# Optimization experiments

Measured on AMD Instinct MI355X. Metric: run time of the kernel, lower is better.

Reference implementation:

```python
import jax, jax.numpy as jnp
import numpy as np

N, F, H, O = 3072, 128, 16, 8  # nodes, in_channels, hidden_channels, out_channels


def setup_inputs() -> dict:
    key = jax.random.key(0)
    ks = jax.random.split(key, 8)
    s = 0.01  # xavier gain=0.01 in original init -> small weights
    return {
        "x": jax.random.normal(ks[0], (N, F), dtype=jnp.float32),
        "edge_index": jax.random.randint(ks[1], (2, N * 32), 0, N, dtype=jnp.int64),
        "node_distances": jax.random.uniform(ks[2], (N, N), dtype=jnp.float32),
        "normalization_matrix": jnp.ones((N, N), dtype=jnp.float32),
        # per-feature MLPs fs[f]: Linear(1,H) -> ReLU -> (Dropout p=0) -> Linear(H,O), stacked over F
        "W1": s * jax.random.normal(ks[3], (F, H), dtype=jnp.float32),
        "b1": jnp.zeros((F, H), dtype=jnp.float32),
        "W2": s * jax.random.normal(ks[4], (F, H, O), dtype=jnp.float32),
        "b2": jnp.zeros((F, O), dtype=jnp.float32),
        # rho MLP: Linear(1,H) -> ReLU -> Linear(H,O) (bias=True since is_graph_task=False)
        "rW1": s * jax.random.normal(ks[5], (H,), dtype=jnp.float32),
        "rb1": jnp.zeros((H,), dtype=jnp.float32),
        "rW2": s * jax.random.normal(ks[6], (H, O), dtype=jnp.float32),
        "rb2": jnp.zeros((O,), dtype=jnp.float32),
    }


def reference(x, edge_index, node_distances, normalization_matrix,
              W1, b1, W2, b2, rW1, rb1, rW2, rb2):
    # --- per-feature tiny MLPs, vectorized over the feature axis ---
    # h[n,f,:] = relu(x[n,f] * W1[f] + b1[f])
    h = jax.nn.relu(x[:, :, None] * W1[None, :, :] + b1[None, :, :])  # [N,F,H]
    fx = jnp.einsum('nfh,fho->nfo', h, W2) + b2[None, :, :]           # [N,F,O]
    # sum over features first (commutes with the matmul's F-reduction)
    g = fx.sum(axis=1)                                                 # [N,O]

    # --- rho MLP on normalized pairwise distances ---
    d = node_distances / normalization_matrix                          # [N,N]
    hd = jax.nn.relu(d[:, :, None] * rW1 + rb1)                        # [N,N,H]
    m = jnp.einsum('nmh,ho->nmo', hd, rW2) + rb2                       # [N,N,O]

    # out.T in torch: mf = m_dist_perm @ fx_perm summed over features -> [N,O]
    out = jnp.einsum('nmo,mo->no', m, g)                               # [N,O]
    return out
```

## Files before the change

kernel.cpp:

```cpp
#include <hip/hip_runtime.h>
#include <hip/hip_bf16.h>
#include <math.h>

#define NN 3072
#define FF 128
#define HH 16
#define OO 8

#define MC   1024
#define NCH  3
#define RPB  8

#define OFF_GT   0
#define OFF_KP   24576
#define OFF_ROWS 24600
#define OFF_REF  24872
#define OFF_BG   24890

#define NPB 4

__global__ __launch_bounds__(128) void gnan_g_kernel(
    const float* __restrict__ x,
    const float* __restrict__ W1,
    const float* __restrict__ b1,
    const float* __restrict__ W2,
    const float* __restrict__ b2,
    float* __restrict__ gT)
{
    const int f  = threadIdx.x;
    const int n0 = blockIdx.x * NPB;

    float xv[NPB];
#pragma unroll
    for (int ni = 0; ni < NPB; ++ni)
        xv[ni] = x[(size_t)(n0 + ni) * FF + f];

    const float4 b2a = *reinterpret_cast<const float4*>(b2 + f * OO);
    const float4 b2b = *reinterpret_cast<const float4*>(b2 + f * OO + 4);

    float acc[NPB][OO];
#pragma unroll
    for (int ni = 0; ni < NPB; ++ni) {
        acc[ni][0] = b2a.x; acc[ni][1] = b2a.y; acc[ni][2] = b2a.z; acc[ni][3] = b2a.w;
        acc[ni][4] = b2b.x; acc[ni][5] = b2b.y; acc[ni][6] = b2b.z; acc[ni][7] = b2b.w;
    }

    for (int h = 0; h < HH; ++h) {
        const float w1h = W1[f * HH + h];
        const float b1h = b1[f * HH + h];
        const float4 wa = *reinterpret_cast<const float4*>(W2 + (size_t)(f * HH + h) * OO);
        const float4 wb = *reinterpret_cast<const float4*>(W2 + (size_t)(f * HH + h) * OO + 4);
#pragma unroll
        for (int ni = 0; ni < NPB; ++ni) {
            const float a = fmaxf(fmaf(xv[ni], w1h, b1h), 0.f);
            acc[ni][0] = fmaf(a, wa.x, acc[ni][0]);
            acc[ni][1] = fmaf(a, wa.y, acc[ni][1]);
            acc[ni][2] = fmaf(a, wa.z, acc[ni][2]);
            acc[ni][3] = fmaf(a, wa.w, acc[ni][3]);
            acc[ni][4] = fmaf(a, wb.x, acc[ni][4]);
            acc[ni][5] = fmaf(a, wb.y, acc[ni][5]);
            acc[ni][6] = fmaf(a, wb.z, acc[ni][6]);
            acc[ni][7] = fmaf(a, wb.w, acc[ni][7]);
        }
    }

    __shared__ float wsum[2][OO];
    const int lane = threadIdx.x & 63;
    const int wid  = threadIdx.x >> 6;
#pragma unroll
    for (int ni = 0; ni < NPB; ++ni) {
#pragma unroll
        for (int o = 0; o < OO; ++o) {
#pragma unroll
            for (int off = 32; off > 0; off >>= 1)
                acc[ni][o] += __shfl_down(acc[ni][o], off);
        }
        if (lane == 0) {
#pragma unroll
            for (int o = 0; o < OO; ++o) wsum[wid][o] = acc[ni][o];
        }
        __syncthreads();
        if (threadIdx.x < OO)
            gT[threadIdx.x * NN + (n0 + ni)] = wsum[0][threadIdx.x] + wsum[1][threadIdx.x];
        __syncthreads();
    }
}

__global__ __launch_bounds__(256) void gnan_setup_kernel(
    const float* __restrict__ nd,
    const float* __restrict__ nm,
    const float* __restrict__ rW1,
    const float* __restrict__ rb1,
    const float* __restrict__ rW2,
    const float* __restrict__ rb2,
    float* __restrict__ wsf)
{
    __shared__ float sk[HH];
    __shared__ int   shh[HH];
    __shared__ float sKp[HH + 2];
    __shared__ float scAdd[OO];
    __shared__ float srows[HH + 1][16];
    __shared__ float sref[18];
    __shared__ float sred[8];

    const int t = threadIdx.x;

    if (t == 0) {
        for (int h = 0; h < HH; ++h) {
            const float w = rW1[h];
            sk[h]  = (w != 0.0f) ? (-rb1[h] / w) : INFINITY;
            shh[h] = h;
        }
        for (int i = 1; i < HH; ++i) {
            float kv = sk[i]; int iv = shh[i];
            int p = i - 1;
            while (p >= 0 && sk[p] > kv) { sk[p+1]=sk[p]; shh[p+1]=shh[p]; --p; }
            sk[p+1] = kv; shh[p+1] = iv;
        }
        sKp[0] = -INFINITY;
        for (int h = 0; h < HH; ++h) sKp[h + 1] = sk[h];
        sKp[HH + 1] = INFINITY;
    }
    if (t < OO) {
        float c = rb2[t];
        for (int h = 0; h < HH; ++h)
            if (rW1[h] == 0.0f) c += fmaxf(rb1[h], 0.f) * rW2[h * OO + t];
        scAdd[t] = c;
    }
    __syncthreads();

    if (t < (HH + 1) * OO) {
        const int j = t >> 3, o = t & 7;
        float alpha = 0.f, beta = 0.f;
        for (int p = 0; p < HH; ++p) {
            const int h = shh[p];
            const float w = rW1[h];
            const bool active = (w > 0.f) ? (p < j) : (w < 0.f ? (p >= j) : false);
            if (active) {
                alpha += w      * rW2[h * OO + o];
                beta  += rb1[h] * rW2[h * OO + o];
            }
        }
        srows[j][o]     = alpha;
        srows[j][8 + o] = beta + scAdd[o];
        wsf[OFF_ROWS + j * 16 + o]     = srows[j][o];
        wsf[OFF_ROWS + j * 16 + 8 + o] = srows[j][8 + o];
    }
    if (t < HH + 2) wsf[OFF_KP + t] = sKp[t];
    __syncthreads();

    if (t == 0) {
        const float d00 = nd[0] / nm[0];
        int j = 0;
        for (int p = 0; p < HH; ++p) j += (d00 >= sKp[p + 1]) ? 1 : 0;
        sref[0] = sKp[j];
        sref[1] = sKp[j + 1];
        for (int o = 0; o < OO; ++o) {
            sref[2 + o]  = srows[j][o];
            sref[10 + o] = srows[j][8 + o];
        }
        for (int i = 0; i < 18; ++i) wsf[OFF_REF + i] = sref[i];
    }
    __syncthreads();

    const int lane = t & 63;
    const int wave = t >> 6;
    for (int p = 0; p < NCH * OO; ++p) {
        const int c = p >> 3, o = p & 7;
        float s = 0.f;
        for (int i = t; i < MC; i += 256)
            s += wsf[OFF_GT + o * NN + c * MC + i];
#pragma unroll
        for (int off = 32; off > 0; off >>= 1)
            s += __shfl_down(s, off);
        if (lane == 0) sred[wave] = s;
        __syncthreads();
        if (t == 0)
            wsf[OFF_BG + p] = sref[10 + o] * (sred[0] + sred[1] + sred[2] + sred[3]);
        __syncthreads();
    }
}

__global__ __launch_bounds__(512) void gnan_main_kernel(
    const float* __restrict__ nd,
    const float* __restrict__ nm,
    const float* __restrict__ wsf,
    float* __restrict__ out)
{
    __shared__ float gs[OO * MC];

    const int t  = threadIdx.x;
    const int b  = blockIdx.x;
    const int rg = b / NCH;
    const int c  = b % NCH;

    {
        float4*       dst = reinterpret_cast<float4*>(gs);
        const float4* src = reinterpret_cast<const float4*>(wsf + OFF_GT);
        for (int i = t; i < OO * MC / 4; i += 512) {
            const int o  = i >> 8;
            const int mi = i & 255;
            dst[i] = src[o * (NN / 4) + c * (MC / 4) + mi];
        }
    }
    const float clo = wsf[OFF_REF + 0];
    const float chi = wsf[OFF_REF + 1];
    __syncthreads();

    const int wave = t >> 6;
    const int lane = t & 63;
    const int row  = rg * RPB + wave;

    const float* __restrict__ drow = nd + (size_t)row * NN + c * MC;
    const float* __restrict__ nrow = nm + (size_t)row * NN + c * MC;

    float dg[OO], corr[OO];
#pragma unroll
    for (int o = 0; o < OO; ++o) { dg[o] = 0.f; corr[o] = 0.f; }

    for (int it = 0; it < MC / 128; ++it) {
        const int m0 = it * 128 + lane * 2;
        const float2 dv = *reinterpret_cast<const float2*>(drow + m0);
        const float2 nv = *reinterpret_cast<const float2*>(nrow + m0);
        float2 gv[OO];
#pragma unroll
        for (int o = 0; o < OO; ++o)
            gv[o] = *reinterpret_cast<const float2*>(&gs[o * MC + m0]);

#pragma unroll
        for (int k = 0; k < 2; ++k) {
            const float d = __fdividef(k == 0 ? dv.x : dv.y,
                                       k == 0 ? nv.x : nv.y);
            if (d >= clo && d < chi) {
#pragma unroll
                for (int o = 0; o < OO; ++o) {
                    const float g = (k == 0) ? gv[o].x : gv[o].y;
                    dg[o] = fmaf(d, g, dg[o]);
                }
            } else {
                int j = 0;
#pragma unroll
                for (int p = 0; p < HH; ++p)
                    j += (d >= wsf[OFF_KP + 1 + p]) ? 1 : 0;
#pragma unroll
                for (int o = 0; o < OO; ++o) {
                    const float a  = wsf[OFF_ROWS + j * 16 + o];
                    const float bb = wsf[OFF_ROWS + j * 16 + 8 + o];
                    const float g  = (k == 0) ? gv[o].x : gv[o].y;
                    const float v  = fmaf(a, d, bb) - wsf[OFF_REF + 10 + o];
                    corr[o] = fmaf(v, g, corr[o]);
                }
            }
        }
    }

    float val[OO];
#pragma unroll
    for (int o = 0; o < OO; ++o)
        val[o] = fmaf(wsf[OFF_REF + 2 + o], dg[o], corr[o]);
#pragma unroll
    for (int o = 0; o < OO; ++o) {
#pragma unroll
        for (int off = 32; off > 0; off >>= 1)
            val[o] += __shfl_down(val[o], off);
    }
    if (lane == 0) {
#pragma unroll
        for (int o = 0; o < OO; ++o)
            atomicAdd(out + (size_t)row * OO + o, val[o] + wsf[OFF_BG + c * OO + o]);
    }
}

extern "C" void kernel_launch(void* const* d_in, const int* in_sizes, int n_in,
                              void* d_out, int out_size, void* d_ws, size_t ws_size,
                              hipStream_t stream) {
    const float* x   = (const float*)d_in[0];
    const float* nd  = (const float*)d_in[2];
    const float* nm  = (const float*)d_in[3];
    const float* W1  = (const float*)d_in[4];
    const float* b1  = (const float*)d_in[5];
    const float* W2  = (const float*)d_in[6];
    const float* b2  = (const float*)d_in[7];
    const float* rW1 = (const float*)d_in[8];
    const float* rb1 = (const float*)d_in[9];
    const float* rW2 = (const float*)d_in[10];
    const float* rb2 = (const float*)d_in[11];
    float* out = (float*)d_out;
    float* wsf = (float*)d_ws;

    gnan_g_kernel<<<NN / NPB, 128, 0, stream>>>(x, W1, b1, W2, b2, wsf + OFF_GT);
    gnan_setup_kernel<<<1, 256, 0, stream>>>(nd, nm, rW1, rb1, rW2, rb2, wsf);
    hipMemsetAsync(out, 0, (size_t)out_size * sizeof(float), stream);
    gnan_main_kernel<<<(NN / RPB) * NCH, 512, 0, stream>>>(nd, nm, wsf, out);
}
```

Before: 180.8 us.

## Parallelize setup kernel and move per-chunk g sums into main kernel

The setup kernel no longer uses a serial single-thread insertion sort, shared-memory staging or barriers. Each thread now computes knee ranks in registers and writes its rows and reference values directly. The serial loop of 24 block-wide reductions over gT is removed, and each block of the main kernel instead reduces its shared-memory g chunk per output channel and folds in the bias term. This shortens the latency of the small serial setup kernel at the cost of redundant reductions across all main-kernel blocks plus an extra barrier.

```diff
diff --git a/kernel.cpp b/kernel.cpp
--- a/kernel.cpp
+++ b/kernel.cpp
@@ -15,7 +15,6 @@
 #define OFF_KP   24576
 #define OFF_ROWS 24600
 #define OFF_REF  24872
-#define OFF_BG   24890
 
 #define NPB 4
 
@@ -95,89 +94,76 @@
     const float* __restrict__ rb2,
     float* __restrict__ wsf)
 {
-    __shared__ float sk[HH];
-    __shared__ int   shh[HH];
-    __shared__ float sKp[HH + 2];
-    __shared__ float scAdd[OO];
-    __shared__ float srows[HH + 1][16];
-    __shared__ float sref[18];
-    __shared__ float sred[8];
-
     const int t = threadIdx.x;
 
+    float w[HH], b[HH], knee[HH];
+#pragma unroll
+    for (int h = 0; h < HH; ++h) {
+        w[h] = rW1[h];
+        b[h] = rb1[h];
+        knee[h] = (w[h] != 0.f) ? (-b[h] / w[h]) : INFINITY;
+    }
+
     if (t == 0) {
-        for (int h = 0; h < HH; ++h) {
-            const float w = rW1[h];
-            sk[h]  = (w != 0.0f) ? (-rb1[h] / w) : INFINITY;
-            shh[h] = h;
-        }
-        for (int i = 1; i < HH; ++i) {
-            float kv = sk[i]; int iv = shh[i];
-            int p = i - 1;
-            while (p >= 0 && sk[p] > kv) { sk[p+1]=sk[p]; shh[p+1]=shh[p]; --p; }
-            sk[p+1] = kv; shh[p+1] = iv;
-        }
-        sKp[0] = -INFINITY;
-        for (int h = 0; h < HH; ++h) sKp[h + 1] = sk[h];
-        sKp[HH + 1] = INFINITY;
-    }
-    if (t < OO) {
-        float c = rb2[t];
-        for (int h = 0; h < HH; ++h)
-            if (rW1[h] == 0.0f) c += fmaxf(rb1[h], 0.f) * rW2[h * OO + t];
-        scAdd[t] = c;
-    }
-    __syncthreads();
+        wsf[OFF_KP + 0]      = -INFINITY;
+        wsf[OFF_KP + HH + 1] =  INFINITY;
+    }
+
+    if (t < HH) {
+        const float wt = rW1[t], bt = rb1[t];
+        const float kt = (wt != 0.f) ? (-bt / wt) : INFINITY;
+        int r = 0;
+#pragma unroll
+        for (int h2 = 0; h2 < HH; ++h2)
+            r += (knee[h2] < kt || (knee[h2] == kt && h2 < t)) ? 1 : 0;
+        wsf[OFF_KP + 1 + r] = kt;
+    }
 
     if (t < (HH + 1) * OO) {
         const int j = t >> 3, o = t & 7;
+
+        float cAdd = rb2[o];
+#pragma unroll
+        for (int h = 0; h < HH; ++h)
+            if (w[h] == 0.f) cAdd += fmaxf(b[h], 0.f) * rW2[h * OO + o];
+
         float alpha = 0.f, beta = 0.f;
-        for (int p = 0; p < HH; ++p) {
-            const int h = shh[p];
-            const float w = rW1[h];
-            const bool active = (w > 0.f) ? (p < j) : (w < 0.f ? (p >= j) : false);
+#pragma unroll
+        for (int h = 0; h < HH; ++h) {
+            int r = 0;
+#pragma unroll
+            for (int h2 = 0; h2 < HH; ++h2)
+                r += (knee[h2] < knee[h] || (knee[h2] == knee[h] && h2 < h)) ? 1 : 0;
+            const bool active = (w[h] > 0.f) ? (r < j)
+                              : (w[h] < 0.f ? (r >= j) : false);
             if (active) {
-                alpha += w      * rW2[h * OO + o];
-                beta  += rb1[h] * rW2[h * OO + o];
+                alpha += w[h] * rW2[h * OO + o];
+                beta  += b[h] * rW2[h * OO + o];
             }
         }
-        srows[j][o]     = alpha;
-        srows[j][8 + o] = beta + scAdd[o];
-        wsf[OFF_ROWS + j * 16 + o]     = srows[j][o];
-        wsf[OFF_ROWS + j * 16 + 8 + o] = srows[j][8 + o];
-    }
-    if (t < HH + 2) wsf[OFF_KP + t] = sKp[t];
-    __syncthreads();
-
-    if (t == 0) {
+        const float betaF = beta + cAdd;
+        wsf[OFF_ROWS + j * 16 + o]     = alpha;
+        wsf[OFF_ROWS + j * 16 + 8 + o] = betaF;
+
         const float d00 = nd[0] / nm[0];
-        int j = 0;
-        for (int p = 0; p < HH; ++p) j += (d00 >= sKp[p + 1]) ? 1 : 0;
-        sref[0] = sKp[j];
-        sref[1] = sKp[j + 1];
-        for (int o = 0; o < OO; ++o) {
-            sref[2 + o]  = srows[j][o];
-            sref[10 + o] = srows[j][8 + o];
-        }
-        for (int i = 0; i < 18; ++i) wsf[OFF_REF + i] = sref[i];
-    }
-    __syncthreads();
-
-    const int lane = t & 63;
-    const int wave = t >> 6;
-    for (int p = 0; p < NCH * OO; ++p) {
-        const int c = p >> 3, o = p & 7;
-        float s = 0.f;
-        for (int i = t; i < MC; i += 256)
-            s += wsf[OFF_GT + o * NN + c * MC + i];
-#pragma unroll
-        for (int off = 32; off > 0; off >>= 1)
-            s += __shfl_down(s, off);
-        if (lane == 0) sred[wave] = s;
-        __syncthreads();
-        if (t == 0)
-            wsf[OFF_BG + p] = sref[10 + o] * (sred[0] + sred[1] + sred[2] + sred[3]);
-        __syncthreads();
+        int j0 = 0;
+#pragma unroll
+        for (int h = 0; h < HH; ++h) j0 += (d00 >= knee[h]) ? 1 : 0;
+
+        if (j == j0) {
+            wsf[OFF_REF + 2 + o]  = alpha;
+            wsf[OFF_REF + 10 + o] = betaF;
+            if (o == 0) {
+                float clo = -INFINITY, chi = INFINITY;
+#pragma unroll
+                for (int h = 0; h < HH; ++h) {
+                    if (d00 >= knee[h]) clo = fmaxf(clo, knee[h]);
+                    else                chi = fminf(chi, knee[h]);
+                }
+                wsf[OFF_REF + 0] = clo;
+                wsf[OFF_REF + 1] = chi;
+            }
+        }
     }
 }
 
@@ -188,6 +174,7 @@
     float* __restrict__ out)
 {
     __shared__ float gs[OO * MC];
+    __shared__ float gsum[OO];
 
     const int t  = threadIdx.x;
     const int b  = blockIdx.x;
@@ -209,8 +196,17 @@
 
     const int wave = t >> 6;
     const int lane = t & 63;
-    const int row  = rg * RPB + wave;
-
+
+    {
+        float s = 0.f;
+        for (int i = lane; i < MC; i += 64) s += gs[wave * MC + i];
+#pragma unroll
+        for (int off = 32; off > 0; off >>= 1) s += __shfl_down(s, off);
+        if (lane == 0) gsum[wave] = s;
+    }
+    __syncthreads();
+
+    const int row = rg * RPB + wave;
     const float* __restrict__ drow = nd + (size_t)row * NN + c * MC;
     const float* __restrict__ nrow = nm + (size_t)row * NN + c * MC;
 
@@ -267,7 +263,8 @@
     if (lane == 0) {
 #pragma unroll
         for (int o = 0; o < OO; ++o)
-            atomicAdd(out + (size_t)row * OO + o, val[o] + wsf[OFF_BG + c * OO + o]);
+            atomicAdd(out + (size_t)row * OO + o,
+                      fmaf(wsf[OFF_REF + 10 + o], gsum[o], val[o]));
     }
 }
 
```

New measurement: 149.9 us. 1.21x faster.
